# Kernel optimization log

Hardware: AMD Instinct MI355X
Metric: run time of the kernel (lower is better)

The kernel has to match this reference:

```python
import math
import jax, jax.numpy as jnp
import numpy as np

B, L, F, H = 16, 1024, 512, 8
D = F // H
FACTOR = 5.0
KEEP_MINLEN = 15.0


def setup_inputs() -> dict:
    key = jax.random.key(0)
    ks = jax.random.split(key, 12)
    inp = {
        "query": jax.random.normal(ks[0], (B, L, F), jnp.float32),
        "key": jax.random.normal(ks[1], (B, L, F), jnp.float32),
        "value": jax.random.normal(ks[2], (B, L, F), jnp.float32),
        "mask": jnp.ones((B, 1, L), jnp.int32),
    }
    s = 0.02
    inp["Wq"] = jax.random.normal(ks[3], (F, F), jnp.float32) * s
    inp["bq"] = jnp.zeros((F,), jnp.float32)
    inp["Wk"] = jax.random.normal(ks[4], (F, F), jnp.float32) * s
    inp["bk"] = jnp.zeros((F,), jnp.float32)
    inp["Wv"] = jax.random.normal(ks[5], (F, F), jnp.float32) * s
    inp["bv"] = jnp.zeros((F,), jnp.float32)
    inp["Wo"] = jax.random.normal(ks[6], (F, F), jnp.float32) * s
    inp["bo"] = jnp.zeros((F,), jnp.float32)
    return inp


def _n_top(Lq: int) -> int:
    if Lq <= KEEP_MINLEN:
        return Lq
    u = int(round(FACTOR * math.ceil(math.log(Lq))))
    return min(u, Lq)


def reference(query, key, value, mask, Wq, bq, Wk, bk, Wv, bv, Wo, bo):
    def proj(x, W, b):
        # torch nn.Linear: x @ W.T + b ; then (B,L,H,D) -> (B,H,L,D)
        return (x @ W.T + b).reshape(B, L, H, D).transpose(0, 2, 1, 3)

    q = proj(query, Wq, bq)
    k = proj(key, Wk, bk)
    v = proj(value, Wv, bv)

    # prob_QK with index=None: full (unscaled) QK to compute sparsity measure M
    scores_full = jnp.einsum('bhqd,bhkd->bhqk', q, k)  # (B,H,L,L)
    M = scores_full.max(-1) - scores_full.mean(-1)      # (B,H,L)
    u = _n_top(L)
    _, idx = jax.lax.top_k(M, u)                        # (B,H,u)

    q_red = jnp.take_along_axis(q, idx[..., None], axis=2)  # (B,H,u,D)
    scores = jnp.einsum('bhud,bhkd->bhuk', q_red, k) / math.sqrt(D)

    neg = (mask == 0)[:, None, :, :]  # (B,1,1,L) broadcasts over heads/queries
    scores = jnp.where(neg, -jnp.inf, scores)
    attn = jax.nn.softmax(scores, axis=-1)
    attn = jnp.where(neg, 0.0, attn)

    ctx_top = jnp.einsum('bhuk,bhkd->bhud', attn, v)   # (B,H,u,D)

    # initial context = mean of V over keys, broadcast to all queries
    context = jnp.broadcast_to(v.mean(axis=2, keepdims=True), (B, H, L, D))
    bi = jnp.arange(B)[:, None, None]
    hi = jnp.arange(H)[None, :, None]
    context = context.at[bi, hi, idx].set(ctx_top)

    x = context.transpose(0, 2, 1, 3).reshape(B, L, H * D)
    return x @ Wo.T + bo
```

## Files before the change

### kernel.cpp

```cpp
#include <hip/hip_runtime.h>
#include <math.h>

#define B_ 16
#define L_ 1024
#define H_ 8
#define U_ 35

typedef float f32x4 __attribute__((ext_vector_type(4)));
typedef short bf16x8 __attribute__((ext_vector_type(8)));

__device__ __forceinline__ unsigned short f2bf(float x) {
    unsigned int u = __float_as_uint(x);
    u += 0x7FFFu + ((u >> 16) & 1u);
    return (unsigned short)(u >> 16);
}
__device__ __forceinline__ float bf2f(unsigned short b) {
    return __uint_as_float(((unsigned int)b) << 16);
}

__device__ __forceinline__ unsigned int cvt_pk_bf16(float a, float b) {
    unsigned int r;
    asm("v_cvt_pk_bf16_f32 %0, %1, %2" : "=v"(r) : "v"(a), "v"(b));
    return r;
}

__device__ __forceinline__ void gl_lds16(const void* g, void* l) {
    __builtin_amdgcn_global_load_lds(
        (const __attribute__((address_space(1))) unsigned int*)g,
        (__attribute__((address_space(3))) unsigned int*)l, 16, 0, 0);
}

#define MFMA(a, b, c) __builtin_amdgcn_mfma_f32_16x16x32_bf16((a), (b), (c), 0, 0, 0)

#define OFF_V      ((size_t)0)
#define OFF_QHI    ((size_t)8388608)
#define OFF_QLO    ((size_t)12582912)
#define OFF_CTXP   OFF_QHI
#define OFF_KHI    ((size_t)16777216)
#define OFF_KLO    ((size_t)20971520)
#define OFF_S      ((size_t)25165824)
#define OFF_WQH    OFF_S
#define OFF_WQL    ((size_t)(OFF_S + 131072))
#define OFF_WKH    ((size_t)(OFF_S + 262144))
#define OFF_WKL    ((size_t)(OFF_S + 393216))
#define OFF_WVH    ((size_t)(OFF_S + 524288))
#define OFF_WVL    ((size_t)(OFF_S + 655360))
#define OFF_M      ((size_t)29753344)
#define OFF_KMEAN  ((size_t)29884416)
#define OFF_VMEAN  ((size_t)29892608)
#define OFF_CTXD   ((size_t)29900800)
#define OFF_IDX    ((size_t)30187520)
#define OFF_OBASE  ((size_t)30192000)

__global__ __launch_bounds__(256) void split_w3(
    const float* __restrict__ Wq, const float* __restrict__ Wk,
    const float* __restrict__ Wv,
    unsigned short* __restrict__ wqh, unsigned short* __restrict__ wql,
    unsigned short* __restrict__ wkh, unsigned short* __restrict__ wkl,
    unsigned short* __restrict__ wvh, unsigned short* __restrict__ wvl)
{
    const int w = blockIdx.x >> 10;
    const int i = (blockIdx.x & 1023) * 256 + threadIdx.x;
    const float* W = (w == 0) ? Wq : (w == 1) ? Wk : Wv;
    unsigned short* hi = (w == 0) ? wqh : (w == 1) ? wkh : wvh;
    unsigned short* lo = (w == 0) ? wql : (w == 1) ? wkl : wvl;
    float x = W[i];
    unsigned short h = f2bf(x);
    hi[i] = h;
    lo[i] = f2bf(x - bf2f(h));
}

__global__ __launch_bounds__(256) void gemm_qkv(
    const float* __restrict__ Aq, const float* __restrict__ Ak,
    const float* __restrict__ Av,
    const unsigned short* __restrict__ wqh, const unsigned short* __restrict__ wql,
    const unsigned short* __restrict__ wkh, const unsigned short* __restrict__ wkl,
    const unsigned short* __restrict__ wvh, const unsigned short* __restrict__ wvl,
    const float* __restrict__ bqp, const float* __restrict__ bkp,
    const float* __restrict__ bvp,
    float* __restrict__ vout,
    unsigned short* __restrict__ qhi_o, unsigned short* __restrict__ qlo_o,
    unsigned short* __restrict__ khi_o, unsigned short* __restrict__ klo_o)
{
    __shared__ __align__(16) unsigned char smem[36864];
    unsigned short (*Ah)[40] = (unsigned short (*)[40])(smem);
    unsigned short (*Al)[40] = (unsigned short (*)[40])(smem + 10240);
    unsigned char* Bh = smem + 20480;
    unsigned char* Bl = smem + 28672;
    float (*Cf)[68] = (float (*)[68])(smem);

    const int z = blockIdx.z;
    const float* A = (z == 0) ? Aq : (z == 1) ? Ak : Av;
    const unsigned short* Whi = (z == 0) ? wqh : (z == 1) ? wkh : wvh;
    const unsigned short* Wlo = (z == 0) ? wql : (z == 1) ? wkl : wvl;
    const float* bias = (z == 0) ? bqp : (z == 1) ? bkp : bvp;
    unsigned short* ohi = (z == 0) ? qhi_o : (z == 1) ? khi_o : nullptr;
    unsigned short* olo = (z == 0) ? qlo_o : (z == 1) ? klo_o : nullptr;

    const int tid = threadIdx.x, lane = tid & 63, wave = tid >> 6;
    const int m0 = blockIdx.x * 128, n0 = blockIdx.y * 128;
    const int wm = (wave >> 1) * 64, wn = (wave & 1) * 64;

    f32x4 zero4 = {0.f, 0.f, 0.f, 0.f};
    f32x4 acc[4][4];
#pragma unroll
    for (int i = 0; i < 4; i++)
#pragma unroll
        for (int j = 0; j < 4; j++) acc[i][j] = zero4;

    const int ar = tid >> 3, ac = (tid & 7) * 4;
    const int kc = (lane >> 4) * 8;
    const int fr = lane & 15;
    const int btr = tid >> 2;
    const int btc = ((tid & 3) ^ ((tid >> 2) & 3)) * 8;
    const int bldsoff = tid * 16;

    float4 areg[4];
#pragma unroll
    for (int p = 0; p < 4; ++p)
        areg[p] = *(const float4*)(A + (size_t)(m0 + ar + p * 32) * 512 + ac);

    for (int k0 = 0; k0 < 512; k0 += 32) {
        if (k0) __syncthreads();
#pragma unroll
        for (int i = 0; i < 2; ++i) {
            size_t gb = (size_t)(n0 + i * 64 + btr) * 512 + k0 + btc;
            gl_lds16(Whi + gb, Bh + i * 4096 + bldsoff);
            gl_lds16(Wlo + gb, Bl + i * 4096 + bldsoff);
        }
#pragma unroll
        for (int p = 0; p < 4; ++p) {
            float4 a4 = areg[p];
            unsigned int h01 = cvt_pk_bf16(a4.x, a4.y);
            unsigned int h23 = cvt_pk_bf16(a4.z, a4.w);
            float r0 = a4.x - __uint_as_float(h01 << 16);
            float r1 = a4.y - __uint_as_float(h01 & 0xFFFF0000u);
            float r2 = a4.z - __uint_as_float(h23 << 16);
            float r3 = a4.w - __uint_as_float(h23 & 0xFFFF0000u);
            unsigned int l01 = cvt_pk_bf16(r0, r1);
            unsigned int l23 = cvt_pk_bf16(r2, r3);
            uint2 hh; hh.x = h01; hh.y = h23;
            uint2 ll; ll.x = l01; ll.y = l23;
            *(uint2*)&Ah[ar + p * 32][ac] = hh;
            *(uint2*)&Al[ar + p * 32][ac] = ll;
        }
        __syncthreads();
        if (k0 + 32 < 512) {
#pragma unroll
            for (int p = 0; p < 4; ++p)
                areg[p] = *(const float4*)(A + (size_t)(m0 + ar + p * 32) * 512 + k0 + 32 + ac);
        }

        bf16x8 ah[4], al[4];
#pragma unroll
        for (int mi = 0; mi < 4; ++mi) {
            int row = wm + mi * 16 + fr;
            ah[mi] = *(bf16x8*)&Ah[row][kc];
            al[mi] = *(bf16x8*)&Al[row][kc];
        }
#pragma unroll
        for (int ni = 0; ni < 4; ++ni) {
            int rn = wn + ni * 16 + fr;
            int bb = rn * 64 + ((kc * 2) ^ ((rn & 3) << 4));
            bf16x8 bh8 = *(bf16x8*)(Bh + bb);
            bf16x8 bl8 = *(bf16x8*)(Bl + bb);
#pragma unroll
            for (int mi = 0; mi < 4; ++mi) {
                acc[mi][ni] = MFMA(ah[mi], bh8, acc[mi][ni]);
                acc[mi][ni] = MFMA(ah[mi], bl8, acc[mi][ni]);
                acc[mi][ni] = MFMA(al[mi], bh8, acc[mi][ni]);
            }
        }
    }

    const int col = lane & 15, rq = (lane >> 4) * 4;
    const int b_ = m0 >> 10;
    const int l0 = m0 & 1023;

#pragma unroll
    for (int half = 0; half < 2; ++half) {
        __syncthreads();
        if ((wave & 1) == half) {
#pragma unroll
            for (int ni = 0; ni < 4; ++ni) {
                float bn = bias[n0 + half * 64 + ni * 16 + col];
#pragma unroll
                for (int mi = 0; mi < 4; ++mi)
#pragma unroll
                    for (int r = 0; r < 4; ++r)
                        Cf[wm + mi * 16 + rq + r][ni * 16 + col] = acc[mi][ni][r] + bn;
            }
        }
        __syncthreads();
        const int h_ = (n0 >> 6) + half;
        const size_t plane = ((size_t)(b_ * H_ + h_) * L_ + l0) * 64;
        if (z == 2) {
            const int r = tid >> 1, d0 = (tid & 1) * 32;
#pragma unroll
            for (int j = 0; j < 8; ++j) {
                float4 val = *(const float4*)&Cf[r][d0 + j * 4];
                *(float4*)(vout + plane + (size_t)r * 64 + d0 + j * 4) = val;
            }
        } else {
            const int r = tid >> 1, d0 = (tid & 1) * 32;
#pragma unroll
            for (int c = 0; c < 4; ++c) {
                float x[8];
#pragma unroll
                for (int j = 0; j < 8; ++j) x[j] = Cf[r][d0 + c * 8 + j];
                unsigned int h01 = cvt_pk_bf16(x[0], x[1]);
                unsigned int h23 = cvt_pk_bf16(x[2], x[3]);
                unsigned int h45 = cvt_pk_bf16(x[4], x[5]);
                unsigned int h67 = cvt_pk_bf16(x[6], x[7]);
                float r0 = x[0] - __uint_as_float(h01 << 16);
                float r1 = x[1] - __uint_as_float(h01 & 0xFFFF0000u);
                float r2 = x[2] - __uint_as_float(h23 << 16);
                float r3 = x[3] - __uint_as_float(h23 & 0xFFFF0000u);
                float r4 = x[4] - __uint_as_float(h45 << 16);
                float r5 = x[5] - __uint_as_float(h45 & 0xFFFF0000u);
                float r6 = x[6] - __uint_as_float(h67 << 16);
                float r7 = x[7] - __uint_as_float(h67 & 0xFFFF0000u);
                uint4 ph; ph.x = h01; ph.y = h23; ph.z = h45; ph.w = h67;
                uint4 pl;
                pl.x = cvt_pk_bf16(r0, r1);
                pl.y = cvt_pk_bf16(r2, r3);
                pl.z = cvt_pk_bf16(r4, r5);
                pl.w = cvt_pk_bf16(r6, r7);
                *(uint4*)(ohi + plane + (size_t)r * 64 + d0 + c * 8) = ph;
                *(uint4*)(olo + plane + (size_t)r * 64 + d0 + c * 8) = pl;
            }
        }
    }
}

__global__ __launch_bounds__(256) void means_fused(
    const unsigned short* __restrict__ khi, const unsigned short* __restrict__ klo,
    const float* __restrict__ v, float* __restrict__ kmean, float* __restrict__ vmean)
{
    const int which = blockIdx.x >> 7;
    const int bh = blockIdx.x & 127;
    const int d = threadIdx.x & 63, g = threadIdx.x >> 6;
    __shared__ float red[4][64];
    float s = 0.f;
    if (which == 0) {
        size_t base = ((size_t)bh * L_ + g * 256) * 64 + d;
#pragma unroll 8
        for (int l = 0; l < 256; l++) {
            size_t o = base + (size_t)l * 64;
            s += bf2f(khi[o]) + bf2f(klo[o]);
        }
    } else {
        const float* p = v + ((size_t)bh * L_ + g * 256) * 64 + d;
#pragma unroll 8
        for (int l = 0; l < 256; l++) s += p[(size_t)l * 64];
    }
    red[g][d] = s;
    __syncthreads();
    if (threadIdx.x < 64) {
        const int dd = threadIdx.x;
        float m = (red[0][dd] + red[1][dd] + red[2][dd] + red[3][dd]) * (1.0f / 1024.0f);
        (which == 0 ? kmean : vmean)[(size_t)bh * 64 + dd] = m;
    }
}

__global__ __launch_bounds__(256) void qk_rowmax_mfma(
    const unsigned short* __restrict__ qhi, const unsigned short* __restrict__ qlo,
    const unsigned short* __restrict__ khi, const unsigned short* __restrict__ klo,
    const float* __restrict__ kmean, float* __restrict__ Mout)
{
    __shared__ unsigned short Qh[64][72], Ql[64][72];
    __shared__ __align__(16) unsigned char Kp[2][2][8192];
    __shared__ float Mred[64][4];
    __shared__ float km[64];
    const int bh = blockIdx.x, q0 = blockIdx.y * 64;
    const int tid = threadIdx.x, lane = tid & 63, wave = tid >> 6;

    if (tid < 64) km[tid] = kmean[bh * 64 + tid];
    {
        int r = tid >> 2, c = (tid & 3) * 16;
        size_t off = ((size_t)bh * L_ + q0 + r) * 64 + c;
        *(uint4*)&Qh[r][c]     = *(const uint4*)(qhi + off);
        *(uint4*)&Qh[r][c + 8] = *(const uint4*)(qhi + off + 8);
        *(uint4*)&Ql[r][c]     = *(const uint4*)(qlo + off);
        *(uint4*)&Ql[r][c + 8] = *(const uint4*)(qlo + off + 8);
    }

    const size_t kb = (size_t)bh * L_ * 64;
    const int srow = tid >> 3;
    const int scol = ((tid & 7) ^ ((tid >> 3) & 7)) * 8;
    const int sdst = tid * 16;

    {
        size_t g0 = kb + (size_t)(srow) * 64 + scol;
        size_t g1 = kb + (size_t)(32 + srow) * 64 + scol;
        gl_lds16(khi + g0, &Kp[0][0][sdst]);
        gl_lds16(khi + g1, &Kp[0][0][4096 + sdst]);
        gl_lds16(klo + g0, &Kp[0][1][sdst]);
        gl_lds16(klo + g1, &Kp[0][1][4096 + sdst]);
    }
    __syncthreads();

    const int fr = lane & 15;
    f32x4 zero4 = {0.f, 0.f, 0.f, 0.f};

    bf16x8 qah[2][4], qal[2][4];
#pragma unroll
    for (int ks = 0; ks < 2; ++ks) {
        int kcol = ks * 32 + (lane >> 4) * 8;
#pragma unroll
        for (int mi = 0; mi < 4; ++mi) {
            qah[ks][mi] = *(bf16x8*)&Qh[mi * 16 + fr][kcol];
            qal[ks][mi] = *(bf16x8*)&Ql[mi * 16 + fr][kcol];
        }
    }

    float rmax[4][4];
#pragma unroll
    for (int mi = 0; mi < 4; ++mi)
#pragma unroll
        for (int r = 0; r < 4; ++r) rmax[mi][r] = -INFINITY;

    const int krow = wave * 16 + fr;
    const int kbase = krow * 128;
    const int kxor = (krow & 7) << 4;

    for (int kt = 0; kt < 16; ++kt) {
        const int cur = kt & 1;
        if (kt < 15) {
            const int nb = cur ^ 1;
            size_t g0 = kb + (size_t)((kt + 1) * 64 + srow) * 64 + scol;
            size_t g1 = g0 + (size_t)32 * 64;
            gl_lds16(khi + g0, &Kp[nb][0][sdst]);
            gl_lds16(khi + g1, &Kp[nb][0][4096 + sdst]);
            gl_lds16(klo + g0, &Kp[nb][1][sdst]);
            gl_lds16(klo + g1, &Kp[nb][1][4096 + sdst]);
        }

        f32x4 acc[4];
#pragma unroll
        for (int mi = 0; mi < 4; ++mi) acc[mi] = zero4;

#pragma unroll
        for (int ks = 0; ks < 2; ++ks) {
            int byte = kbase + (((ks * 32 + (lane >> 4) * 8) * 2) ^ kxor);
            bf16x8 bh8 = *(bf16x8*)&Kp[cur][0][byte];
            bf16x8 bl8 = *(bf16x8*)&Kp[cur][1][byte];
#pragma unroll
            for (int mi = 0; mi < 4; ++mi) {
                acc[mi] = MFMA(qah[ks][mi], bh8, acc[mi]);
                acc[mi] = MFMA(qah[ks][mi], bl8, acc[mi]);
                acc[mi] = MFMA(qal[ks][mi], bh8, acc[mi]);
            }
        }
#pragma unroll
        for (int mi = 0; mi < 4; ++mi)
#pragma unroll
            for (int r = 0; r < 4; ++r)
                rmax[mi][r] = fmaxf(rmax[mi][r], acc[mi][r]);

        __syncthreads();
    }

#pragma unroll
    for (int mi = 0; mi < 4; ++mi)
#pragma unroll
        for (int r = 0; r < 4; ++r) {
            float v = rmax[mi][r];
            v = fmaxf(v, __shfl_xor(v, 1));
            v = fmaxf(v, __shfl_xor(v, 2));
            v = fmaxf(v, __shfl_xor(v, 4));
            v = fmaxf(v, __shfl_xor(v, 8));
            rmax[mi][r] = v;
        }
    if ((lane & 15) == 0) {
        int quad = lane >> 4;
#pragma unroll
        for (int mi = 0; mi < 4; ++mi)
#pragma unroll
            for (int r = 0; r < 4; ++r)
                Mred[mi * 16 + quad * 4 + r][wave] = rmax[mi][r];
    }
    __syncthreads();
    if (tid < 64) {
        float mx = fmaxf(fmaxf(Mred[tid][0], Mred[tid][1]),
                         fmaxf(Mred[tid][2], Mred[tid][3]));
        float dot = 0.f;
#pragma unroll 4
        for (int d = 0; d < 64; ++d)
            dot = fmaf(bf2f(Qh[tid][d]) + bf2f(Ql[tid][d]), km[d], dot);
        Mout[(size_t)bh * L_ + q0 + tid] = mx - dot;
    }
}

__global__ __launch_bounds__(256) void topk35(
    const float* __restrict__ Min, int* __restrict__ idx_out)
{
    const int bh = blockIdx.x;
    const int tid = threadIdx.x;
    __shared__ float vals[1024];
    __shared__ float wv[4];
    __shared__ int wi[4];
    for (int i = tid; i < 1024; i += 256) vals[i] = Min[(size_t)bh * 1024 + i];
    __syncthreads();
    for (int it = 0; it < U_; ++it) {
        float bv = -INFINITY; int bi = 1 << 30;
        for (int i = tid; i < 1024; i += 256) {
            float x = vals[i];
            if (x > bv) { bv = x; bi = i; }
        }
#pragma unroll
        for (int off = 32; off; off >>= 1) {
            float ov = __shfl_down(bv, off);
            int   oi = __shfl_down(bi, off);
            if (ov > bv || (ov == bv && oi < bi)) { bv = ov; bi = oi; }
        }
        if ((tid & 63) == 0) { wv[tid >> 6] = bv; wi[tid >> 6] = bi; }
        __syncthreads();
        if (tid == 0) {
#pragma unroll
            for (int w = 1; w < 4; ++w) {
                if (wv[w] > bv || (wv[w] == bv && wi[w] < bi)) { bv = wv[w]; bi = wi[w]; }
            }
            idx_out[bh * U_ + it] = bi;
            vals[bi] = -INFINITY;
        }
        __syncthreads();
    }
}

__global__ __launch_bounds__(256) void scores_red(
    const unsigned short* __restrict__ qhi, const unsigned short* __restrict__ qlo,
    const unsigned short* __restrict__ khi, const unsigned short* __restrict__ klo,
    const int* __restrict__ idx, const int* __restrict__ mask,
    float* __restrict__ S)
{
    __shared__ float Qs[64][36];
    __shared__ float Ks[64][68];
    const int bh = blockIdx.x;
    const int b = bh >> 3;
    const int tid = threadIdx.x;
    const int tk = tid & 63, tg = tid >> 6;

    for (int t = tid; t < 36 * 64; t += 256) {
        int u = t >> 6, d = t & 63;
        float val = 0.f;
        if (u < U_) {
            int l = idx[bh * U_ + u];
            size_t off = ((size_t)bh * L_ + l) * 64 + d;
            val = bf2f(qhi[off]) + bf2f(qlo[off]);
        }
        Qs[d][u] = val;
    }

    const size_t kb = (size_t)bh * L_ * 64;
    const int sr = tid >> 2, sc = (tid & 3) * 16;
    float acc[9];
    const int kt0 = blockIdx.y * 2;
    for (int ki = 0; ki < 2; ++ki) {
        int kt = kt0 + ki;
        if (ki) __syncthreads();
        {
            size_t off = kb + (size_t)(kt * 64 + sr) * 64 + sc;
            uint4 h0 = *(const uint4*)(khi + off);
            uint4 h1 = *(const uint4*)(khi + off + 8);
            uint4 l0 = *(const uint4*)(klo + off);
            uint4 l1 = *(const uint4*)(klo + off + 8);
            unsigned short hv[16], lv[16];
            *(uint4*)hv = h0; *(uint4*)(hv + 8) = h1;
            *(uint4*)lv = l0; *(uint4*)(lv + 8) = l1;
#pragma unroll
            for (int i = 0; i < 16; ++i)
                Ks[sc + i][sr] = bf2f(hv[i]) + bf2f(lv[i]);
        }
        __syncthreads();
#pragma unroll
        for (int j = 0; j < 9; j++) acc[j] = 0.f;
#pragma unroll 4
        for (int d = 0; d < 64; ++d) {
            float kv = Ks[d][tk];
#pragma unroll
            for (int j = 0; j < 9; j++) acc[j] = fmaf(Qs[d][tg + 4 * j], kv, acc[j]);
        }
        const int kcol = kt * 64 + tk;
        const bool msk = (mask[b * L_ + kcol] == 0);
#pragma unroll
        for (int j = 0; j < 9; j++) {
            int u = tg + 4 * j;
            if (u < U_)
                S[((size_t)bh * U_ + u) * 1024 + kcol] = msk ? -INFINITY : acc[j] * 0.125f;
        }
    }
}

__global__ __launch_bounds__(256) void softmax_rows(float* __restrict__ S)
{
    const size_t base = (size_t)blockIdx.x * 1024;
    const int tid = threadIdx.x;
    __shared__ float redm[4];
    __shared__ float reds[4];
    float4 v = *(const float4*)(S + base + tid * 4);
    float mx = fmaxf(fmaxf(v.x, v.y), fmaxf(v.z, v.w));
#pragma unroll
    for (int off = 32; off; off >>= 1) mx = fmaxf(mx, __shfl_down(mx, off));
    if ((tid & 63) == 0) redm[tid >> 6] = mx;
    __syncthreads();
    mx = fmaxf(fmaxf(redm[0], redm[1]), fmaxf(redm[2], redm[3]));
    float e0 = __expf(v.x - mx), e1 = __expf(v.y - mx);
    float e2 = __expf(v.z - mx), e3 = __expf(v.w - mx);
    float s = e0 + e1 + e2 + e3;
#pragma unroll
    for (int off = 32; off; off >>= 1) s += __shfl_down(s, off);
    if ((tid & 63) == 0) reds[tid >> 6] = s;
    __syncthreads();
    s = reds[0] + reds[1] + reds[2] + reds[3];
    const float inv = 1.0f / s;
    float4 o; o.x = e0 * inv; o.y = e1 * inv; o.z = e2 * inv; o.w = e3 * inv;
    *(float4*)(S + base + tid * 4) = o;
}

__global__ __launch_bounds__(256) void ctx_partial(
    const float* __restrict__ S, const float* __restrict__ v,
    float* __restrict__ ctxp)
{
    __shared__ float Vs[128][68];
    __shared__ float Wt[36][128];
    const int bh = blockIdx.x, kc = blockIdx.y;
    const int tid = threadIdx.x;
    const int td = tid & 63, tg = tid >> 6;
    const int lr = tid >> 2, lc0 = (tid & 3) * 16;

    const float* vbase = v + ((size_t)bh * L_ + kc * 128) * 64;
    const float* Sbase = S + (size_t)bh * U_ * 1024 + kc * 128;

#pragma unroll
    for (int hh = 0; hh < 2; ++hh) {
        int row = lr + hh * 64;
        const float* src = vbase + (size_t)row * 64 + lc0;
        *(float4*)&Vs[row][lc0 + 0]  = *(const float4*)(src + 0);
        *(float4*)&Vs[row][lc0 + 4]  = *(const float4*)(src + 4);
        *(float4*)&Vs[row][lc0 + 8]  = *(const float4*)(src + 8);
        *(float4*)&Vs[row][lc0 + 12] = *(const float4*)(src + 12);
    }
    for (int t = tid; t < 36 * 128; t += 256) {
        int u = t >> 7, kk = t & 127;
        Wt[u][kk] = (u < U_) ? Sbase[(size_t)u * 1024 + kk] : 0.f;
    }
    __syncthreads();

    float acc[9];
#pragma unroll
    for (int j = 0; j < 9; j++) acc[j] = 0.f;
#pragma unroll 2
    for (int kk = 0; kk < 128; ++kk) {
        float vv = Vs[kk][td];
#pragma unroll
        for (int j = 0; j < 9; j++) acc[j] = fmaf(Wt[tg + 4 * j][kk], vv, acc[j]);
    }
#pragma unroll
    for (int j = 0; j < 9; j++) {
        int u = tg + 4 * j;
        if (u < U_)
            ctxp[((size_t)(kc * 128 + bh) * 36 + u) * 64 + td] = acc[j];
    }
}

__global__ __launch_bounds__(256) void ctx_reduce_diff(
    const float* __restrict__ ctxp, const float* __restrict__ vmean,
    float* __restrict__ ctxd)
{
    const int i = blockIdx.x * 256 + threadIdx.x;
    const int d = i & 63;
    const int rest = i >> 6;
    const int u = rest % U_;
    const int bh = rest / U_;
    float s = 0.f;
#pragma unroll
    for (int kc = 0; kc < 8; ++kc)
        s += ctxp[((size_t)(kc * 128 + bh) * 36 + u) * 64 + d];
    ctxd[i] = s - vmean[(size_t)bh * 64 + d];
}

__global__ __launch_bounds__(256) void vmean_proj(
    const float* __restrict__ vmean, const float* __restrict__ Wo,
    const float* __restrict__ bo, float* __restrict__ obase)
{
    const int b = blockIdx.x >> 3, n0 = (blockIdx.x & 7) * 64;
    const int tid = threadIdx.x;
    __shared__ float xbar[512];
    __shared__ float psum[64][5];
    for (int i = tid; i < 512; i += 256)
        xbar[i] = vmean[(size_t)(b * 8 + (i >> 6)) * 64 + (i & 63)];
    __syncthreads();
    const int n = n0 + (tid >> 2), fq = (tid & 3) * 128;
    float s = 0.f;
    for (int f = 0; f < 128; f += 4) {
        float4 w = *(const float4*)(Wo + (size_t)n * 512 + fq + f);
        s += xbar[fq + f] * w.x + xbar[fq + f + 1] * w.y +
             xbar[fq + f + 2] * w.z + xbar[fq + f + 3] * w.w;
    }
    psum[tid >> 2][tid & 3] = s;
    __syncthreads();
    if (tid < 64)
        obase[(size_t)b * 512 + n0 + tid] =
            psum[tid][0] + psum[tid][1] + psum[tid][2] + psum[tid][3] + bo[n0 + tid];
}

__global__ void broadcast_out(const float* __restrict__ obase, float* __restrict__ out)
{
    const size_t e = ((size_t)blockIdx.x * 256 + threadIdx.x) * 4;
    const int n = (int)(e & 511);
    const int b = (int)(e >> 19);
    *(float4*)(out + e) = *(const float4*)(obase + (b << 9) + n);
}

__global__ __launch_bounds__(128) void delta_out(
    const float* __restrict__ ctxd, const int* __restrict__ idx,
    const float* __restrict__ Wo, float* __restrict__ out)
{
    const int bh = blockIdx.x, b = bh >> 3, h = bh & 7;
    const int tid = threadIdx.x;
    const int n = blockIdx.y * 128 + tid;
    __shared__ float sd[U_][64];
    __shared__ int ls[U_];
    if (tid < U_) ls[tid] = idx[bh * U_ + tid];
    for (int t = tid; t < U_ * 64; t += 128)
        sd[t >> 6][t & 63] = ctxd[(size_t)bh * U_ * 64 + t];

    float4 w[16];
    const float* wp = Wo + (size_t)n * 512 + h * 64;
#pragma unroll
    for (int jc = 0; jc < 16; ++jc) w[jc] = *(const float4*)(wp + jc * 4);
    __syncthreads();

    for (int u = 0; u < U_; ++u) {
        float acc = 0.f;
#pragma unroll
        for (int jc = 0; jc < 16; ++jc) {
            float4 dv = *(const float4*)&sd[u][jc * 4];
            acc = fmaf(dv.w, w[jc].w, fmaf(dv.z, w[jc].z,
                  fmaf(dv.y, w[jc].y, fmaf(dv.x, w[jc].x, acc))));
        }
        atomicAdd(out + ((size_t)b * L_ + ls[u]) * 512 + n, acc);
    }
}

extern "C" void kernel_launch(void* const* d_in, const int* in_sizes, int n_in,
                              void* d_out, int out_size, void* d_ws, size_t ws_size,
                              hipStream_t stream)
{
    (void)in_sizes; (void)n_in; (void)out_size; (void)ws_size;
    const float* query = (const float*)d_in[0];
    const float* key   = (const float*)d_in[1];
    const float* value = (const float*)d_in[2];
    const int*   mask  = (const int*)d_in[3];
    const float* Wq = (const float*)d_in[4];
    const float* bq = (const float*)d_in[5];
    const float* Wk = (const float*)d_in[6];
    const float* bk = (const float*)d_in[7];
    const float* Wv = (const float*)d_in[8];
    const float* bvp = (const float*)d_in[9];
    const float* Wo = (const float*)d_in[10];
    const float* bo = (const float*)d_in[11];
    float* out = (float*)d_out;

    float* ws = (float*)d_ws;
    float* v      = ws + OFF_V;
    unsigned short* q_hi = (unsigned short*)(ws + OFF_QHI);
    unsigned short* q_lo = (unsigned short*)(ws + OFF_QLO);
    unsigned short* k_hi = (unsigned short*)(ws + OFF_KHI);
    unsigned short* k_lo = (unsigned short*)(ws + OFF_KLO);
    float* ctxp   = ws + OFF_CTXP;
    float* S      = ws + OFF_S;
    float* Marr   = ws + OFF_M;
    float* kmean  = ws + OFF_KMEAN;
    float* vmean  = ws + OFF_VMEAN;
    float* ctxd   = ws + OFF_CTXD;
    int*   idx    = (int*)(ws + OFF_IDX);
    float* obase  = ws + OFF_OBASE;
    unsigned short* wqh = (unsigned short*)(ws + OFF_WQH);
    unsigned short* wql = (unsigned short*)(ws + OFF_WQL);
    unsigned short* wkh = (unsigned short*)(ws + OFF_WKH);
    unsigned short* wkl = (unsigned short*)(ws + OFF_WKL);
    unsigned short* wvh = (unsigned short*)(ws + OFF_WVH);
    unsigned short* wvl = (unsigned short*)(ws + OFF_WVL);

    split_w3<<<3072, 256, 0, stream>>>(Wq, Wk, Wv, wqh, wql, wkh, wkl, wvh, wvl);

    gemm_qkv<<<dim3(128, 4, 3), 256, 0, stream>>>(
        query, key, value,
        wqh, wql, wkh, wkl, wvh, wvl,
        bq, bk, bvp,
        v, q_hi, q_lo, k_hi, k_lo);

    means_fused<<<256, 256, 0, stream>>>(k_hi, k_lo, v, kmean, vmean);
    vmean_proj<<<128, 256, 0, stream>>>(vmean, Wo, bo, obase);

    qk_rowmax_mfma<<<dim3(128, 16), 256, 0, stream>>>(q_hi, q_lo, k_hi, k_lo, kmean, Marr);
    topk35<<<128, 256, 0, stream>>>(Marr, idx);

    scores_red<<<dim3(128, 8), 256, 0, stream>>>(q_hi, q_lo, k_hi, k_lo, idx, mask, S);
    softmax_rows<<<B_ * H_ * U_, 256, 0, stream>>>(S);
    ctx_partial<<<dim3(128, 8), 256, 0, stream>>>(S, v, ctxp);
    ctx_reduce_diff<<<1120, 256, 0, stream>>>(ctxp, vmean, ctxd);

    broadcast_out<<<8192, 256, 0, stream>>>(obase, out);
    delta_out<<<dim3(128, 4), 128, 0, stream>>>(ctxd, idx, Wo, out);
}
```

Measured before the change: 435.4 us.

## Double query tile per block in QK rowmax and re-swizzle GEMM B LDS layout

The QK row-max kernel now handles 128 query rows per block instead of 64. Each K tile loaded into LDS is therefore reused across two query sub-tiles, which halves K global traffic and the grid size. Separately, the QKV projection GEMM gets a new rotation-based LDS swizzle for the weight tiles, meant to reduce bank conflicts. The larger tile doubles the Q fragment registers and the LDS footprint, which may lower occupancy.

Result: no change. 442.5 us (+1.6%).

```diff
diff --git a/kernel.cpp b/kernel.cpp
--- a/kernel.cpp
+++ b/kernel.cpp
@@ -110,9 +110,10 @@
 
     const int ar = tid >> 3, ac = (tid & 7) * 4;
     const int kc = (lane >> 4) * 8;
+    const int q4 = lane >> 4;
     const int fr = lane & 15;
     const int btr = tid >> 2;
-    const int btc = ((tid & 3) ^ ((tid >> 2) & 3)) * 8;
+    const int btc = ((((tid & 3) - btr - (btr >> 2)) & 3)) * 8;
     const int bldsoff = tid * 16;
 
     float4 areg[4];
@@ -161,7 +162,8 @@
 #pragma unroll
         for (int ni = 0; ni < 4; ++ni) {
             int rn = wn + ni * 16 + fr;
-            int bb = rn * 64 + ((kc * 2) ^ ((rn & 3) << 4));
+            int sl = (q4 + rn + (rn >> 2)) & 3;
+            int bb = rn * 64 + sl * 16;
             bf16x8 bh8 = *(bf16x8*)(Bh + bb);
             bf16x8 bl8 = *(bf16x8*)(Bl + bb);
 #pragma unroll
@@ -268,21 +270,25 @@
     const unsigned short* __restrict__ khi, const unsigned short* __restrict__ klo,
     const float* __restrict__ kmean, float* __restrict__ Mout)
 {
-    __shared__ unsigned short Qh[64][72], Ql[64][72];
+    __shared__ unsigned short Qh[128][72], Ql[128][72];
     __shared__ __align__(16) unsigned char Kp[2][2][8192];
-    __shared__ float Mred[64][4];
+    __shared__ float Mred[128][4];
     __shared__ float km[64];
-    const int bh = blockIdx.x, q0 = blockIdx.y * 64;
+    const int bh = blockIdx.x, q0 = blockIdx.y * 128;
     const int tid = threadIdx.x, lane = tid & 63, wave = tid >> 6;
 
     if (tid < 64) km[tid] = kmean[bh * 64 + tid];
     {
-        int r = tid >> 2, c = (tid & 3) * 16;
+        int r = tid >> 1, c = (tid & 1) * 32;
         size_t off = ((size_t)bh * L_ + q0 + r) * 64 + c;
-        *(uint4*)&Qh[r][c]     = *(const uint4*)(qhi + off);
-        *(uint4*)&Qh[r][c + 8] = *(const uint4*)(qhi + off + 8);
-        *(uint4*)&Ql[r][c]     = *(const uint4*)(qlo + off);
-        *(uint4*)&Ql[r][c + 8] = *(const uint4*)(qlo + off + 8);
+        *(uint4*)&Qh[r][c]      = *(const uint4*)(qhi + off);
+        *(uint4*)&Qh[r][c + 8]  = *(const uint4*)(qhi + off + 8);
+        *(uint4*)&Qh[r][c + 16] = *(const uint4*)(qhi + off + 16);
+        *(uint4*)&Qh[r][c + 24] = *(const uint4*)(qhi + off + 24);
+        *(uint4*)&Ql[r][c]      = *(const uint4*)(qlo + off);
+        *(uint4*)&Ql[r][c + 8]  = *(const uint4*)(qlo + off + 8);
+        *(uint4*)&Ql[r][c + 16] = *(const uint4*)(qlo + off + 16);
+        *(uint4*)&Ql[r][c + 24] = *(const uint4*)(qlo + off + 24);
     }
 
     const size_t kb = (size_t)bh * L_ * 64;
@@ -303,22 +309,26 @@
     const int fr = lane & 15;
     f32x4 zero4 = {0.f, 0.f, 0.f, 0.f};
 
-    bf16x8 qah[2][4], qal[2][4];
-#pragma unroll
-    for (int ks = 0; ks < 2; ++ks) {
-        int kcol = ks * 32 + (lane >> 4) * 8;
-#pragma unroll
-        for (int mi = 0; mi < 4; ++mi) {
-            qah[ks][mi] = *(bf16x8*)&Qh[mi * 16 + fr][kcol];
-            qal[ks][mi] = *(bf16x8*)&Ql[mi * 16 + fr][kcol];
-        }
-    }
-
-    float rmax[4][4];
-#pragma unroll
-    for (int mi = 0; mi < 4; ++mi)
-#pragma unroll
-        for (int r = 0; r < 4; ++r) rmax[mi][r] = -INFINITY;
+    bf16x8 qah[2][2][4], qal[2][2][4];
+#pragma unroll
+    for (int qt = 0; qt < 2; ++qt)
+#pragma unroll
+        for (int ks = 0; ks < 2; ++ks) {
+            int kcol = ks * 32 + (lane >> 4) * 8;
+#pragma unroll
+            for (int mi = 0; mi < 4; ++mi) {
+                qah[qt][ks][mi] = *(bf16x8*)&Qh[qt * 64 + mi * 16 + fr][kcol];
+                qal[qt][ks][mi] = *(bf16x8*)&Ql[qt * 64 + mi * 16 + fr][kcol];
+            }
+        }
+
+    float rmax[2][4][4];
+#pragma unroll
+    for (int qt = 0; qt < 2; ++qt)
+#pragma unroll
+        for (int mi = 0; mi < 4; ++mi)
+#pragma unroll
+            for (int r = 0; r < 4; ++r) rmax[qt][mi][r] = -INFINITY;
 
     const int krow = wave * 16 + fr;
     const int kbase = krow * 128;
@@ -336,52 +346,63 @@
             gl_lds16(klo + g1, &Kp[nb][1][4096 + sdst]);
         }
 
-        f32x4 acc[4];
-#pragma unroll
-        for (int mi = 0; mi < 4; ++mi) acc[mi] = zero4;
-
+        bf16x8 kfh[2], kfl[2];
 #pragma unroll
         for (int ks = 0; ks < 2; ++ks) {
             int byte = kbase + (((ks * 32 + (lane >> 4) * 8) * 2) ^ kxor);
-            bf16x8 bh8 = *(bf16x8*)&Kp[cur][0][byte];
-            bf16x8 bl8 = *(bf16x8*)&Kp[cur][1][byte];
-#pragma unroll
-            for (int mi = 0; mi < 4; ++mi) {
-                acc[mi] = MFMA(qah[ks][mi], bh8, acc[mi]);
-                acc[mi] = MFMA(qah[ks][mi], bl8, acc[mi]);
-                acc[mi] = MFMA(qal[ks][mi], bh8, acc[mi]);
+            kfh[ks] = *(bf16x8*)&Kp[cur][0][byte];
+            kfl[ks] = *(bf16x8*)&Kp[cur][1][byte];
+        }
+
+#pragma unroll
+        for (int qt = 0; qt < 2; ++qt) {
+            f32x4 acc[4];
+#pragma unroll
+            for (int mi = 0; mi < 4; ++mi) acc[mi] = zero4;
+#pragma unroll
+            for (int ks = 0; ks < 2; ++ks) {
+#pragma unroll
+                for (int mi = 0; mi < 4; ++mi) {
+                    acc[mi] = MFMA(qah[qt][ks][mi], kfh[ks], acc[mi]);
+                    acc[mi] = MFMA(qah[qt][ks][mi], kfl[ks], acc[mi]);
+                    acc[mi] = MFMA(qal[qt][ks][mi], kfh[ks], acc[mi]);
+                }
             }
-        }
+#pragma unroll
+            for (int mi = 0; mi < 4; ++mi)
+#pragma unroll
+                for (int r = 0; r < 4; ++r)
+                    rmax[qt][mi][r] = fmaxf(rmax[qt][mi][r], acc[mi][r]);
+        }
+
+        __syncthreads();
+    }
+
+#pragma unroll
+    for (int qt = 0; qt < 2; ++qt)
 #pragma unroll
         for (int mi = 0; mi < 4; ++mi)
 #pragma unroll
-            for (int r = 0; r < 4; ++r)
-                rmax[mi][r] = fmaxf(rmax[mi][r], acc[mi][r]);
-
-        __syncthreads();
-    }
-
-#pragma unroll
-    for (int mi = 0; mi < 4; ++mi)
-#pragma unroll
-        for (int r = 0; r < 4; ++r) {
-            float v = rmax[mi][r];
-            v = fmaxf(v, __shfl_xor(v, 1));
-            v = fmaxf(v, __shfl_xor(v, 2));
-            v = fmaxf(v, __shfl_xor(v, 4));
-            v = fmaxf(v, __shfl_xor(v, 8));
-            rmax[mi][r] = v;
-        }
+            for (int r = 0; r < 4; ++r) {
+                float v = rmax[qt][mi][r];
+                v = fmaxf(v, __shfl_xor(v, 1));
+                v = fmaxf(v, __shfl_xor(v, 2));
+                v = fmaxf(v, __shfl_xor(v, 4));
+                v = fmaxf(v, __shfl_xor(v, 8));
+                rmax[qt][mi][r] = v;
+            }
     if ((lane & 15) == 0) {
         int quad = lane >> 4;
 #pragma unroll
-        for (int mi = 0; mi < 4; ++mi)
-#pragma unroll
-            for (int r = 0; r < 4; ++r)
-                Mred[mi * 16 + quad * 4 + r][wave] = rmax[mi][r];
-    }
-    __syncthreads();
-    if (tid < 64) {
+        for (int qt = 0; qt < 2; ++qt)
+#pragma unroll
+            for (int mi = 0; mi < 4; ++mi)
+#pragma unroll
+                for (int r = 0; r < 4; ++r)
+                    Mred[qt * 64 + mi * 16 + quad * 4 + r][wave] = rmax[qt][mi][r];
+    }
+    __syncthreads();
+    if (tid < 128) {
         float mx = fmaxf(fmaxf(Mred[tid][0], Mred[tid][1]),
                          fmaxf(Mred[tid][2], Mred[tid][3]));
         float dot = 0.f;
@@ -695,7 +716,7 @@
     means_fused<<<256, 256, 0, stream>>>(k_hi, k_lo, v, kmean, vmean);
     vmean_proj<<<128, 256, 0, stream>>>(vmean, Wo, bo, obase);
 
-    qk_rowmax_mfma<<<dim3(128, 16), 256, 0, stream>>>(q_hi, q_lo, k_hi, k_lo, kmean, Marr);
+    qk_rowmax_mfma<<<dim3(128, 8), 256, 0, stream>>>(q_hi, q_lo, k_hi, k_lo, kmean, Marr);
     topk35<<<128, 256, 0, stream>>>(Marr, idx);
 
     scores_red<<<dim3(128, 8), 256, 0, stream>>>(q_hi, q_lo, k_hi, k_lo, idx, mask, S);
```

## Replace iterative argmax top-k with radix-select and change LDS swizzle for B tiles

Applied to the files above, without the earlier changes.

The top-35 selection per (batch, head) row moves from 35 sequential block-wide argmax passes, each with two barriers, to a 4-pass 8-bit radix select over order-preserving float keys. Elements above the threshold are then emitted with an atomic counter, and ties are filled in index order. Output order within the 35 indices is no longer sorted, which is fine if the downstream scatter does not depend on order. The LDS swizzle for the projection GEMM's B tiles also changes from XOR to a rotational pattern, aimed at reducing bank conflicts.

Result: slower. 490.0 us (+12.6%).

```diff
diff --git a/kernel.cpp b/kernel.cpp
--- a/kernel.cpp
+++ b/kernel.cpp
@@ -110,9 +110,10 @@
 
     const int ar = tid >> 3, ac = (tid & 7) * 4;
     const int kc = (lane >> 4) * 8;
+    const int q4 = lane >> 4;
     const int fr = lane & 15;
     const int btr = tid >> 2;
-    const int btc = ((tid & 3) ^ ((tid >> 2) & 3)) * 8;
+    const int btc = ((((tid & 3) - btr - (btr >> 2)) & 3)) * 8;
     const int bldsoff = tid * 16;
 
     float4 areg[4];
@@ -161,7 +162,8 @@
 #pragma unroll
         for (int ni = 0; ni < 4; ++ni) {
             int rn = wn + ni * 16 + fr;
-            int bb = rn * 64 + ((kc * 2) ^ ((rn & 3) << 4));
+            int sl = (q4 + rn + (rn >> 2)) & 3;
+            int bb = rn * 64 + sl * 16;
             bf16x8 bh8 = *(bf16x8*)(Bh + bb);
             bf16x8 bl8 = *(bf16x8*)(Bl + bb);
 #pragma unroll
@@ -397,34 +399,51 @@
 {
     const int bh = blockIdx.x;
     const int tid = threadIdx.x;
-    __shared__ float vals[1024];
-    __shared__ float wv[4];
-    __shared__ int wi[4];
-    for (int i = tid; i < 1024; i += 256) vals[i] = Min[(size_t)bh * 1024 + i];
-    __syncthreads();
-    for (int it = 0; it < U_; ++it) {
-        float bv = -INFINITY; int bi = 1 << 30;
+    __shared__ unsigned int keys[1024];
+    __shared__ int hist[256];
+    __shared__ unsigned int s_prefix;
+    __shared__ int s_rank;
+    __shared__ int s_cnt;
+
+    for (int i = tid; i < 1024; i += 256) {
+        unsigned int u = __float_as_uint(Min[(size_t)bh * 1024 + i]);
+        keys[i] = (u & 0x80000000u) ? ~u : (u | 0x80000000u);
+    }
+    if (tid == 0) { s_prefix = 0u; s_rank = U_; s_cnt = 0; }
+
+    for (int p = 0; p < 4; ++p) {
+        __syncthreads();
+        hist[tid] = 0;
+        __syncthreads();
+        const int sh = 24 - 8 * p;
+        const unsigned int pref = s_prefix;
         for (int i = tid; i < 1024; i += 256) {
-            float x = vals[i];
-            if (x > bv) { bv = x; bi = i; }
-        }
-#pragma unroll
-        for (int off = 32; off; off >>= 1) {
-            float ov = __shfl_down(bv, off);
-            int   oi = __shfl_down(bi, off);
-            if (ov > bv || (ov == bv && oi < bi)) { bv = ov; bi = oi; }
-        }
-        if ((tid & 63) == 0) { wv[tid >> 6] = bv; wi[tid >> 6] = bi; }
+            unsigned int k = keys[i];
+            bool m = (p == 0) || ((k >> (sh + 8)) == pref);
+            if (m) atomicAdd(&hist[(k >> sh) & 255], 1);
+        }
         __syncthreads();
         if (tid == 0) {
-#pragma unroll
-            for (int w = 1; w < 4; ++w) {
-                if (wv[w] > bv || (wv[w] == bv && wi[w] < bi)) { bv = wv[w]; bi = wi[w]; }
-            }
-            idx_out[bh * U_ + it] = bi;
-            vals[bi] = -INFINITY;
-        }
-        __syncthreads();
+            int r = s_rank, cum = 0, b = 255;
+            for (; b > 0; --b) { cum += hist[b]; if (cum >= r) break; }
+            if (cum < r) cum += hist[0];
+            s_rank = r - (cum - hist[b]);
+            s_prefix = (pref << 8) | (unsigned int)b;
+        }
+    }
+    __syncthreads();
+    const unsigned int T = s_prefix;
+    for (int i = tid; i < 1024; i += 256) {
+        if (keys[i] > T) {
+            int pos = atomicAdd(&s_cnt, 1);
+            idx_out[bh * U_ + pos] = i;
+        }
+    }
+    __syncthreads();
+    if (tid == 0) {
+        int pos = s_cnt;
+        for (int i = 0; i < 1024 && pos < U_; ++i)
+            if (keys[i] == T) idx_out[bh * U_ + pos++] = i;
     }
 }
 
```
